# Optimization experiments

Measured on AMD Instinct MI355X. Metric: run time of the kernel, lower is better.

Reference implementation:

```python
import jax, jax.numpy as jnp
import numpy as np

D_MODEL = 1024
N_HEADS = 16
HEAD_DIM = D_MODEL // N_HEADS
SEQ_LEN = 2048
D_FF = 4 * D_MODEL
LCC_SCALE = 0.1
LN_EPS = 1e-5
NORM_EPS = 1e-12  # F.normalize eps


def _layer_norm(x, g, b):
    mu = jnp.mean(x, axis=-1, keepdims=True)
    var = jnp.mean(jnp.square(x - mu), axis=-1, keepdims=True)
    return (x - mu) * jax.lax.rsqrt(var + LN_EPS) * g + b


def setup_inputs() -> dict:
    key = jax.random.key(0)
    ks = jax.random.split(key, 8)
    s = 0.02  # weight init scale
    return {
        "x": jax.random.normal(ks[0], (SEQ_LEN, D_MODEL), jnp.float32),
        "lcc_values": jax.random.uniform(ks[1], (SEQ_LEN,), jnp.float32),
        "w_qkv": jax.random.normal(ks[2], (D_MODEL, 3 * D_MODEL), jnp.float32) * s,
        "b_qkv": jnp.zeros((3 * D_MODEL,), jnp.float32),
        "w_out": jax.random.normal(ks[3], (D_MODEL, D_MODEL), jnp.float32) * s,
        "b_out": jnp.zeros((D_MODEL,), jnp.float32),
        "ln1_g": jnp.ones((D_MODEL,), jnp.float32),
        "ln1_b": jnp.zeros((D_MODEL,), jnp.float32),
        "ln2_g": jnp.ones((D_MODEL,), jnp.float32),
        "ln2_b": jnp.zeros((D_MODEL,), jnp.float32),
        "w_ff1": jax.random.normal(ks[4], (D_MODEL, D_FF), jnp.float32) * s,
        "b_ff1": jnp.zeros((D_FF,), jnp.float32),
        "w_ff2": jax.random.normal(ks[5], (D_FF, D_MODEL), jnp.float32) * s,
        "b_ff2": jnp.zeros((D_MODEL,), jnp.float32),
    }


def reference(x, lcc_values, w_qkv, b_qkv, w_out, b_out, ln1_g, ln1_b,
              ln2_g, ln2_b, w_ff1, b_ff1, w_ff2, b_ff2):
    L = x.shape[0]
    scaling = HEAD_DIM ** -0.5

    normed = _layer_norm(x, ln1_g, ln1_b)
    qkv = normed @ w_qkv + b_qkv                      # [L, 3D]
    qkv = qkv.reshape(L, 3, N_HEADS, HEAD_DIM)
    q = jnp.transpose(qkv[:, 0], (1, 0, 2))           # [H, L, d]
    k = jnp.transpose(qkv[:, 1], (1, 0, 2))
    v = jnp.transpose(qkv[:, 2], (1, 0, 2))

    # cosine attention: L2-normalize q, k
    q = q / jnp.maximum(jnp.linalg.norm(q, axis=-1, keepdims=True), NORM_EPS)
    k = k / jnp.maximum(jnp.linalg.norm(k, axis=-1, keepdims=True), NORM_EPS)
    q = q * scaling

    scores = jnp.einsum('hld,hmd->hlm', q, k)         # [H, L, L]
    bias = (lcc_values[:, None] + lcc_values[None, :]) * 0.5 * LCC_SCALE
    scores = jnp.clip(scores + bias[None], -10.0, 10.0)
    probs = jax.nn.softmax(scores, axis=-1)

    attn = jnp.einsum('hlm,hmd->hld', probs, v)       # [H, L, d]
    attn = jnp.transpose(attn, (1, 0, 2)).reshape(L, D_MODEL)
    x = x + (attn @ w_out + b_out)

    normed2 = _layer_norm(x, ln2_g, ln2_b)
    h = jax.nn.gelu(normed2 @ w_ff1 + b_ff1, approximate=False)
    x = x + (h @ w_ff2 + b_ff2)
    return x
```

## Files before the change

kernel.cpp:

```cpp
#include <hip/hip_runtime.h>
#include <hip/hip_bf16.h>

#define D_MODEL 1024
#define SEQ 2048
#define NH 16
#define HD 64
#define DFF 4096

typedef __attribute__((ext_vector_type(8))) __bf16 bf16x8;
typedef __attribute__((ext_vector_type(4))) float f32x4;

__device__ __forceinline__ unsigned short f2bf(float f) {
    union { float f; unsigned u; } v; v.f = f;
    unsigned r = v.u + 0x7fffu + ((v.u >> 16) & 1u);
    return (unsigned short)(r >> 16);
}
__device__ __forceinline__ unsigned pack2(float a, float b) {
    return (unsigned)f2bf(a) | ((unsigned)f2bf(b) << 16);
}
__device__ __forceinline__ float bf2f(unsigned short u) {
    union { unsigned u; float f; } v; v.u = ((unsigned)u) << 16;
    return v.f;
}
__device__ __forceinline__ bf16x8 ld_frag(const unsigned short* p) {
    union { uint4 u; bf16x8 b; } c;
    c.u = *(const uint4*)p;
    return c.b;
}
__device__ __forceinline__ void load16(const float* p, float* v) {
#pragma unroll
    for (int i = 0; i < 4; i++) {
        float4 f = ((const float4*)p)[i];
        v[4*i+0]=f.x; v[4*i+1]=f.y; v[4*i+2]=f.z; v[4*i+3]=f.w;
    }
}

typedef __attribute__((address_space(3))) unsigned lds_u32;
typedef const __attribute__((address_space(1))) unsigned glob_u32;
__device__ __forceinline__ void gl_lds16(const unsigned short* g, unsigned short* l) {
    __builtin_amdgcn_global_load_lds((glob_u32*)g, (lds_u32*)l, 16, 0, 0);
}

#define MFMA16(a,b,c) __builtin_amdgcn_mfma_f32_16x16x32_bf16(a,b,c,0,0,0)

__global__ __launch_bounds__(256) void wcast_t(const float* __restrict__ W,
                                               unsigned short* __restrict__ Wt,
                                               int K, int N) {
    __shared__ unsigned short lt[64][72];
    int t = threadIdx.x;
    int nb = blockIdx.x, kb = blockIdx.y;
    int r = t >> 2, c0 = (t & 3) << 4;
    const float* src = W + (size_t)(kb*64 + r) * N + nb*64 + c0;
    float4 f0 = ((const float4*)src)[0];
    float4 f1 = ((const float4*)src)[1];
    float4 f2 = ((const float4*)src)[2];
    float4 f3 = ((const float4*)src)[3];
    unsigned* dst = (unsigned*)&lt[r][c0];
    dst[0]=pack2(f0.x,f0.y); dst[1]=pack2(f0.z,f0.w);
    dst[2]=pack2(f1.x,f1.y); dst[3]=pack2(f1.z,f1.w);
    dst[4]=pack2(f2.x,f2.y); dst[5]=pack2(f2.z,f2.w);
    dst[6]=pack2(f3.x,f3.y); dst[7]=pack2(f3.z,f3.w);
    __syncthreads();
    int n_ = t >> 2, k0 = (t & 3) << 4;
    unsigned obuf[8];
#pragma unroll
    for (int i = 0; i < 8; i++)
        obuf[i] = (unsigned)lt[k0 + 2*i][n_] | ((unsigned)lt[k0 + 2*i + 1][n_] << 16);
    unsigned short* out = Wt + (size_t)(nb*64 + n_) * K + kb*64 + k0;
    ((uint4*)out)[0] = *(uint4*)&obuf[0];
    ((uint4*)out)[1] = *(uint4*)&obuf[4];
}

__global__ __launch_bounds__(256) void ln_kernel(const float* __restrict__ x,
                                                 const float* __restrict__ g,
                                                 const float* __restrict__ b,
                                                 unsigned short* __restrict__ out) {
    int row = blockIdx.x, t = threadIdx.x;
    float4 v = ((const float4*)(x + (size_t)row * D_MODEL))[t];
    float s  = v.x + v.y + v.z + v.w;
    float sq = v.x*v.x + v.y*v.y + v.z*v.z + v.w*v.w;
#pragma unroll
    for (int m = 1; m < 64; m <<= 1) { s += __shfl_xor(s, m, 64); sq += __shfl_xor(sq, m, 64); }
    __shared__ float ls[4], lq[4];
    int wave = t >> 6, lane = t & 63;
    if (lane == 0) { ls[wave] = s; lq[wave] = sq; }
    __syncthreads();
    s  = ls[0]+ls[1]+ls[2]+ls[3];
    sq = lq[0]+lq[1]+lq[2]+lq[3];
    float mu  = s * (1.0f / D_MODEL);
    float var = sq * (1.0f / D_MODEL) - mu * mu;
    float rs  = rsqrtf(var + 1e-5f);
    int c = t * 4;
    float y0 = (v.x - mu) * rs * g[c+0] + b[c+0];
    float y1 = (v.y - mu) * rs * g[c+1] + b[c+1];
    float y2 = (v.z - mu) * rs * g[c+2] + b[c+2];
    float y3 = (v.w - mu) * rs * g[c+3] + b[c+3];
    unsigned* o = (unsigned*)(out + (size_t)row * D_MODEL + c);
    o[0] = pack2(y0, y1); o[1] = pack2(y2, y3);
}

template<int NP>
__global__ __launch_bounds__(256) void reduce_k(const float* __restrict__ res,
                                                const float* __restrict__ bias,
                                                const unsigned short* __restrict__ parts,
                                                float* __restrict__ out,
                                                int MN, int Ndiv4) {
    int i = blockIdx.x * 256 + threadIdx.x;
    float4 r = ((const float4*)res)[i];
    float4 b = ((const float4*)bias)[i & (Ndiv4 - 1)];
    r.x += b.x; r.y += b.y; r.z += b.z; r.w += b.w;
#pragma unroll
    for (int p = 0; p < NP; p++) {
        ushort4 u = ((const ushort4*)(parts + (size_t)p * MN))[i];
        r.x += bf2f(u.x); r.y += bf2f(u.y); r.z += bf2f(u.z); r.w += bf2f(u.w);
    }
    ((float4*)out)[i] = r;
}

template<int TM, int TN, int SPLITK, int GELU, int RES, int OUTBF, int PART>
__global__ __launch_bounds__(256) void gemm_bt(const unsigned short* __restrict__ A,
                                               const unsigned short* __restrict__ Bt,
                                               const float* __restrict__ bias,
                                               const float* __restrict__ res,
                                               void* __restrict__ C,
                                               int M, int N, int K) {
    constexpr int AI = TM / 32;
    constexpr int BI = TN / 32;
    constexpr int MI = TM / 32;
    constexpr int NI = TN / 32;
    constexpr int HALF = (TM + TN) * 64;
    __shared__ unsigned short smem[2 * HALF];
    int t = threadIdx.x;
    int bn = blockIdx.x, bm = blockIdx.y;
    int kz = (SPLITK > 1) ? blockIdx.z : 0;
    int KS = K / SPLITK;
    int K0 = kz * KS;
    int wave = t >> 6, lane = t & 63;
    int quad = lane >> 4, lr = lane & 15;

    const unsigned short* pa[AI];
    int aoff[AI];
#pragma unroll
    for (int i = 0; i < AI; i++) {
        int rl = wave*(TM/4) + i*8 + (lane >> 3);
        int ss = (lane & 7) ^ (rl & 7);
        pa[i] = A + (size_t)(bm*TM + rl) * K + K0 + ss*8;
        aoff[i] = (wave*(TM/4) + i*8) * 64;
    }
    const unsigned short* pb[BI];
    int boff[BI];
#pragma unroll
    for (int i = 0; i < BI; i++) {
        int rl = wave*(TN/4) + i*8 + (lane >> 3);
        int ss = (lane & 7) ^ (rl & 7);
        pb[i] = Bt + (size_t)(bn*TN + rl) * K + K0 + ss*8;
        boff[i] = TM*64 + (wave*(TN/4) + i*8) * 64;
    }

    int wr = (wave >> 1) * (TM/2), wc = (wave & 1) * (TN/2);
    int foA[2][MI], foB[2][NI];
#pragma unroll
    for (int i = 0; i < MI; i++) {
        int row = wr + i*16 + lr;
        foA[0][i] = row*64 + ((quad     ^ (row & 7)))*8;
        foA[1][i] = row*64 + (((quad+4) ^ (row & 7)))*8;
    }
#pragma unroll
    for (int j = 0; j < NI; j++) {
        int row = wc + j*16 + lr;
        foB[0][j] = TM*64 + row*64 + ((quad     ^ (row & 7)))*8;
        foB[1][j] = TM*64 + row*64 + (((quad+4) ^ (row & 7)))*8;
    }

    f32x4 z = {0.f, 0.f, 0.f, 0.f};
    f32x4 acc[MI][NI];
#pragma unroll
    for (int i = 0; i < MI; i++)
#pragma unroll
        for (int j = 0; j < NI; j++) acc[i][j] = z;

#pragma unroll
    for (int i = 0; i < AI; i++) gl_lds16(pa[i], smem + aoff[i]);
#pragma unroll
    for (int i = 0; i < BI; i++) gl_lds16(pb[i], smem + boff[i]);

    int bo = 0;
    for (int kk = 0; kk < KS; kk += 64) {
        __syncthreads();
        if (kk + 64 < KS) {
            int nb = bo ^ HALF;
#pragma unroll
            for (int i = 0; i < AI; i++) gl_lds16(pa[i] + kk + 64, smem + nb + aoff[i]);
#pragma unroll
            for (int i = 0; i < BI; i++) gl_lds16(pb[i] + kk + 64, smem + nb + boff[i]);
        }
#pragma unroll
        for (int h = 0; h < 2; h++) {
            bf16x8 af[MI], bfr[NI];
#pragma unroll
            for (int i = 0; i < MI; i++) af[i]  = ld_frag(smem + bo + foA[h][i]);
#pragma unroll
            for (int j = 0; j < NI; j++) bfr[j] = ld_frag(smem + bo + foB[h][j]);
#pragma unroll
            for (int i = 0; i < MI; i++)
#pragma unroll
                for (int j = 0; j < NI; j++)
                    acc[i][j] = MFMA16(af[i], bfr[j], acc[i][j]);
        }
        bo ^= HALF;
    }

    if (PART) {
        unsigned short* P = (unsigned short*)C + (size_t)kz * M * N;
#pragma unroll
        for (int i = 0; i < MI; i++)
#pragma unroll
            for (int j = 0; j < NI; j++) {
                int row0 = bm*TM + wr + i*16 + quad*4;
                int col  = bn*TN + wc + j*16 + lr;
#pragma unroll
                for (int r = 0; r < 4; r++)
                    P[(size_t)(row0 + r) * N + col] = f2bf(acc[i][j][r]);
            }
    } else {
#pragma unroll
        for (int i = 0; i < MI; i++)
#pragma unroll
            for (int j = 0; j < NI; j++) {
                int row0 = bm*TM + wr + i*16 + quad*4;
                int col  = bn*TN + wc + j*16 + lr;
                float bv = bias[col];
#pragma unroll
                for (int r = 0; r < 4; r++) {
                    float v = acc[i][j][r] + bv;
                    if (RES)  v += res[(size_t)(row0 + r) * N + col];
                    if (GELU) v = 0.5f * v * (1.0f + erff(v * 0.70710678118654752f));
                    if (OUTBF) ((unsigned short*)C)[(size_t)(row0 + r) * N + col] = f2bf(v);
                    else       ((float*)C)[(size_t)(row0 + r) * N + col] = v;
                }
            }
    }
}

__global__ __launch_bounds__(256) void qkv_post(const float* __restrict__ qkv,
                                                unsigned short* __restrict__ qn,
                                                unsigned short* __restrict__ kn,
                                                unsigned short* __restrict__ vt) {
    __shared__ unsigned short lv[64][72];
    int h = blockIdx.x, lb = blockIdx.y;
    int t = threadIdx.x;
    int lloc = t >> 2, seg = (t & 3) << 4;
    int lg = lb*64 + lloc;
    const float* row = qkv + (size_t)lg * 3072;
    float vq[16], vk[16], vv[16];
    load16(row + h*64 + seg, vq);
    load16(row + 1024 + h*64 + seg, vk);
    load16(row + 2048 + h*64 + seg, vv);
    float sq = 0.f, sk = 0.f;
#pragma unroll
    for (int i = 0; i < 16; i++) { sq += vq[i]*vq[i]; sk += vk[i]*vk[i]; }
    sq += __shfl_xor(sq, 1, 64); sq += __shfl_xor(sq, 2, 64);
    sk += __shfl_xor(sk, 1, 64); sk += __shfl_xor(sk, 2, 64);
    float scq = 0.125f / fmaxf(sqrtf(sq), 1e-12f);
    float sck = 1.0f   / fmaxf(sqrtf(sk), 1e-12f);
    unsigned* oq = (unsigned*)(qn + ((size_t)h*SEQ + lg)*HD + seg);
    unsigned* ok = (unsigned*)(kn + ((size_t)h*SEQ + lg)*HD + seg);
#pragma unroll
    for (int i = 0; i < 8; i++) {
        oq[i] = pack2(vq[2*i]*scq, vq[2*i+1]*scq);
        ok[i] = pack2(vk[2*i]*sck, vk[2*i+1]*sck);
    }
    unsigned* lvp = (unsigned*)&lv[lloc][seg];
#pragma unroll
    for (int i = 0; i < 8; i++) lvp[i] = pack2(vv[2*i], vv[2*i+1]);
    __syncthreads();
    int dloc = t >> 2, l0 = (t & 3) << 4;
    unsigned obuf[8];
#pragma unroll
    for (int i = 0; i < 8; i++)
        obuf[i] = (unsigned)lv[l0 + 2*i][dloc] | ((unsigned)lv[l0 + 2*i + 1][dloc] << 16);
    unsigned short* ov = vt + ((size_t)h*HD + dloc)*SEQ + lb*64 + l0;
    ((uint4*)ov)[0] = *(uint4*)&obuf[0];
    ((uint4*)ov)[1] = *(uint4*)&obuf[4];
}

__global__ __launch_bounds__(256) void attn_kernel(const unsigned short* __restrict__ qn,
                                                   const unsigned short* __restrict__ kn,
                                                   const unsigned short* __restrict__ vt,
                                                   const float* __restrict__ lcc,
                                                   unsigned short* __restrict__ attn) {
    __shared__ unsigned short lQ[64][72];
    __shared__ unsigned short lK[64][72];
    __shared__ unsigned short lV[64][72];
    __shared__ unsigned short lP[64][72];
    __shared__ float lL[SEQ];
    int h = blockIdx.x, qb = blockIdx.y;
    int t = threadIdx.x;
    int rl = t >> 2, c0 = (t & 3) << 4;
    const unsigned short* pq = qn + ((size_t)h*SEQ + qb*64 + rl)*HD + c0;
    *(uint4*)&lQ[rl][c0]     = ((const uint4*)pq)[0];
    *(uint4*)&lQ[rl][c0 + 8] = ((const uint4*)pq)[1];
    for (int i = t; i < SEQ; i += 256) lL[i] = 0.05f * lcc[i];
    __syncthreads();
    int wave = t >> 6, lane = t & 63, quad = lane >> 4, lr = lane & 15;
    float lqv[4];
#pragma unroll
    for (int r = 0; r < 4; r++) lqv[r] = lL[qb*64 + wave*16 + quad*4 + r];
    bf16x8 aq0 = ld_frag(&lQ[wave*16 + lr][quad*8]);
    bf16x8 aq1 = ld_frag(&lQ[wave*16 + lr][32 + quad*8]);
    f32x4 z = {0.f, 0.f, 0.f, 0.f};
    f32x4 oacc[4]; oacc[0]=z; oacc[1]=z; oacc[2]=z; oacc[3]=z;
    float den[4] = {0.f, 0.f, 0.f, 0.f};

    for (int kb = 0; kb < SEQ/64; kb++) {
        __syncthreads();
        const unsigned short* pk = kn + ((size_t)h*SEQ + kb*64 + rl)*HD + c0;
        uint4 k0v = ((const uint4*)pk)[0], k1v = ((const uint4*)pk)[1];
        const unsigned short* pv = vt + ((size_t)h*HD + rl)*SEQ + kb*64 + c0;
        uint4 v0v = ((const uint4*)pv)[0], v1v = ((const uint4*)pv)[1];
        *(uint4*)&lK[rl][c0]     = k0v; *(uint4*)&lK[rl][c0 + 8] = k1v;
        *(uint4*)&lV[rl][c0]     = v0v; *(uint4*)&lV[rl][c0 + 8] = v1v;
        __syncthreads();
#pragma unroll
        for (int j = 0; j < 4; j++) {
            bf16x8 b0 = ld_frag(&lK[j*16 + lr][quad*8]);
            bf16x8 b1 = ld_frag(&lK[j*16 + lr][32 + quad*8]);
            f32x4 s = z;
            s = MFMA16(aq0, b0, s);
            s = MFMA16(aq1, b1, s);
            float lm = lL[kb*64 + j*16 + lr];
#pragma unroll
            for (int r = 0; r < 4; r++) {
                float sv = s[r] + lqv[r] + lm;
                sv = fminf(fmaxf(sv, -10.f), 10.f);
                float p = __expf(sv);
                den[r] += p;
                lP[wave*16 + quad*4 + r][j*16 + lr] = f2bf(p);
            }
        }
        bf16x8 ap0 = ld_frag(&lP[wave*16 + lr][quad*8]);
        bf16x8 ap1 = ld_frag(&lP[wave*16 + lr][32 + quad*8]);
#pragma unroll
        for (int j2 = 0; j2 < 4; j2++) {
            bf16x8 b0 = ld_frag(&lV[j2*16 + lr][quad*8]);
            bf16x8 b1 = ld_frag(&lV[j2*16 + lr][32 + quad*8]);
            oacc[j2] = MFMA16(ap0, b0, oacc[j2]);
            oacc[j2] = MFMA16(ap1, b1, oacc[j2]);
        }
    }
#pragma unroll
    for (int r = 0; r < 4; r++)
#pragma unroll
        for (int m = 1; m < 16; m <<= 1) den[r] += __shfl_xor(den[r], m, 64);
#pragma unroll
    for (int j2 = 0; j2 < 4; j2++)
#pragma unroll
        for (int r = 0; r < 4; r++) {
            float ov = oacc[j2][r] / den[r];
            int rowg = qb*64 + wave*16 + quad*4 + r;
            int colg = h*64 + j2*16 + lr;
            attn[(size_t)rowg * D_MODEL + colg] = f2bf(ov);
        }
}

extern "C" void kernel_launch(void* const* d_in, const int* in_sizes, int n_in,
                              void* d_out, int out_size, void* d_ws, size_t ws_size,
                              hipStream_t stream) {
    const float* x      = (const float*)d_in[0];
    const float* lcc    = (const float*)d_in[1];
    const float* w_qkv  = (const float*)d_in[2];
    const float* b_qkv  = (const float*)d_in[3];
    const float* w_out  = (const float*)d_in[4];
    const float* b_out  = (const float*)d_in[5];
    const float* ln1_g  = (const float*)d_in[6];
    const float* ln1_b  = (const float*)d_in[7];
    const float* ln2_g  = (const float*)d_in[8];
    const float* ln2_b  = (const float*)d_in[9];
    const float* w_ff1  = (const float*)d_in[10];
    const float* b_ff1  = (const float*)d_in[11];
    const float* w_ff2  = (const float*)d_in[12];
    const float* b_ff2  = (const float*)d_in[13];

    char* ws = (char*)d_ws;
    unsigned short* wtq  = (unsigned short*)(ws);
    unsigned short* wto  = (unsigned short*)(ws + 6291456);
    unsigned short* wtf1 = (unsigned short*)(ws + 8388608);
    unsigned short* wtf2 = (unsigned short*)(ws + 16777216);
    unsigned short* xn   = (unsigned short*)(ws + 25165824);
    float*          qkvb = (float*)(ws + 29360128);
    float*          x1   = (float*)(ws + 29360128);
    unsigned short* hbuf = (unsigned short*)(ws + 37748736);
    unsigned short* pOP  = (unsigned short*)(ws + 37748736);
    unsigned short* qnb  = (unsigned short*)(ws + 54525952);
    unsigned short* knb  = (unsigned short*)(ws + 58720256);
    unsigned short* vtb  = (unsigned short*)(ws + 62914560);
    unsigned short* pFF2 = (unsigned short*)(ws);
    unsigned short* attnb = xn;
    unsigned short* x2n  = qnb;
    float* outp = (float*)d_out;

    wcast_t<<<dim3(48, 16), 256, 0, stream>>>(w_qkv, wtq, 1024, 3072);
    wcast_t<<<dim3(16, 16), 256, 0, stream>>>(w_out, wto, 1024, 1024);
    wcast_t<<<dim3(64, 16), 256, 0, stream>>>(w_ff1, wtf1, 1024, 4096);
    wcast_t<<<dim3(16, 64), 256, 0, stream>>>(w_ff2, wtf2, 4096, 1024);
    ln_kernel<<<SEQ, 256, 0, stream>>>(x, ln1_g, ln1_b, xn);
    gemm_bt<128,64,1,0,0,0,0><<<dim3(48, 16), 256, 0, stream>>>(xn, wtq, b_qkv, nullptr, qkvb, SEQ, 3072, 1024);
    qkv_post<<<dim3(16, 32), 256, 0, stream>>>(qkvb, qnb, knb, vtb);
    attn_kernel<<<dim3(16, 32), 256, 0, stream>>>(qnb, knb, vtb, lcc, attnb);
    gemm_bt<128,64,2,0,0,0,1><<<dim3(16, 16, 2), 256, 0, stream>>>(attnb, wto, nullptr, nullptr, pOP, SEQ, 1024, 1024);
    reduce_k<2><<<SEQ*D_MODEL/1024, 256, 0, stream>>>(x, b_out, pOP, x1, SEQ*D_MODEL, D_MODEL/4);
    ln_kernel<<<SEQ, 256, 0, stream>>>(x1, ln2_g, ln2_b, x2n);
    gemm_bt<128,64,1,1,0,1,0><<<dim3(64, 16), 256, 0, stream>>>(x2n, wtf1, b_ff1, nullptr, hbuf, SEQ, 4096, 1024);
    gemm_bt<128,64,4,0,0,0,1><<<dim3(16, 16, 4), 256, 0, stream>>>(hbuf, wtf2, nullptr, nullptr, pFF2, SEQ, 1024, 4096);
    reduce_k<4><<<SEQ*D_MODEL/1024, 256, 0, stream>>>(x1, b_ff2, pFF2, outp, SEQ*D_MODEL, D_MODEL/4);
}
```

Baseline: 294.5 us.

## Split attention over key dimension and add combine kernel

Attention now splits the key sequence into two halves across a third grid dimension. Each block writes unnormalized fp32 numerators and row denominators to workspace, and a new combine kernel sums the halves, normalizes and writes bf16 output. This doubles the number of attention blocks to improve GPU occupancy, at the cost of extra workspace traffic and one more launch. GEMM and reduce templates are wrapped in named non-template kernels, with no intended speed effect.

```diff
diff --git a/kernel.cpp b/kernel.cpp
--- a/kernel.cpp
+++ b/kernel.cpp
@@ -100,11 +100,11 @@
 }
 
 template<int NP>
-__global__ __launch_bounds__(256) void reduce_k(const float* __restrict__ res,
-                                                const float* __restrict__ bias,
-                                                const unsigned short* __restrict__ parts,
-                                                float* __restrict__ out,
-                                                int MN, int Ndiv4) {
+__device__ __forceinline__ void reduce_body(const float* __restrict__ res,
+                                            const float* __restrict__ bias,
+                                            const unsigned short* __restrict__ parts,
+                                            float* __restrict__ out,
+                                            int MN, int Ndiv4) {
     int i = blockIdx.x * 256 + threadIdx.x;
     float4 r = ((const float4*)res)[i];
     float4 b = ((const float4*)bias)[i & (Ndiv4 - 1)];
@@ -116,14 +116,24 @@
     }
     ((float4*)out)[i] = r;
 }
+__global__ __launch_bounds__(256) void reduce_op(const float* res, const float* bias,
+                                                 const unsigned short* parts, float* out,
+                                                 int MN, int Ndiv4) {
+    reduce_body<2>(res, bias, parts, out, MN, Ndiv4);
+}
+__global__ __launch_bounds__(256) void reduce_ff2(const float* res, const float* bias,
+                                                  const unsigned short* parts, float* out,
+                                                  int MN, int Ndiv4) {
+    reduce_body<4>(res, bias, parts, out, MN, Ndiv4);
+}
 
 template<int TM, int TN, int SPLITK, int GELU, int RES, int OUTBF, int PART>
-__global__ __launch_bounds__(256) void gemm_bt(const unsigned short* __restrict__ A,
-                                               const unsigned short* __restrict__ Bt,
-                                               const float* __restrict__ bias,
-                                               const float* __restrict__ res,
-                                               void* __restrict__ C,
-                                               int M, int N, int K) {
+__device__ __forceinline__ void gemm_body(const unsigned short* __restrict__ A,
+                                          const unsigned short* __restrict__ Bt,
+                                          const float* __restrict__ bias,
+                                          const float* __restrict__ res,
+                                          void* __restrict__ C,
+                                          int M, int N, int K) {
     constexpr int AI = TM / 32;
     constexpr int BI = TN / 32;
     constexpr int MI = TM / 32;
@@ -240,6 +250,23 @@
                 }
             }
     }
+}
+
+__global__ __launch_bounds__(256) void k_gemm_qkv(const unsigned short* A, const unsigned short* Bt,
+                                                  const float* bias, float* C, int M, int N, int K) {
+    gemm_body<128,64,1,0,0,0,0>(A, Bt, bias, nullptr, C, M, N, K);
+}
+__global__ __launch_bounds__(256) void k_gemm_op(const unsigned short* A, const unsigned short* Bt,
+                                                 unsigned short* C, int M, int N, int K) {
+    gemm_body<128,64,2,0,0,0,1>(A, Bt, nullptr, nullptr, C, M, N, K);
+}
+__global__ __launch_bounds__(256) void k_gemm_ff1(const unsigned short* A, const unsigned short* Bt,
+                                                  const float* bias, unsigned short* C, int M, int N, int K) {
+    gemm_body<128,64,1,1,0,1,0>(A, Bt, bias, nullptr, C, M, N, K);
+}
+__global__ __launch_bounds__(256) void k_gemm_ff2(const unsigned short* A, const unsigned short* Bt,
+                                                  unsigned short* C, int M, int N, int K) {
+    gemm_body<128,64,4,0,0,0,1>(A, Bt, nullptr, nullptr, C, M, N, K);
 }
 
 __global__ __launch_bounds__(256) void qkv_post(const float* __restrict__ qkv,
@@ -284,39 +311,45 @@
     ((uint4*)ov)[1] = *(uint4*)&obuf[4];
 }
 
+#define KSPLIT 2
+#define KTILES (SEQ / 64 / KSPLIT)
 __global__ __launch_bounds__(256) void attn_kernel(const unsigned short* __restrict__ qn,
                                                    const unsigned short* __restrict__ kn,
                                                    const unsigned short* __restrict__ vt,
                                                    const float* __restrict__ lcc,
-                                                   unsigned short* __restrict__ attn) {
+                                                   float* __restrict__ num_ws,
+                                                   float* __restrict__ den_ws) {
     __shared__ unsigned short lQ[64][72];
     __shared__ unsigned short lK[64][72];
     __shared__ unsigned short lV[64][72];
     __shared__ unsigned short lP[64][72];
-    __shared__ float lL[SEQ];
-    int h = blockIdx.x, qb = blockIdx.y;
+    __shared__ float lL[SEQ / KSPLIT];
+    int h = blockIdx.x, qb = blockIdx.y, kz = blockIdx.z;
     int t = threadIdx.x;
     int rl = t >> 2, c0 = (t & 3) << 4;
     const unsigned short* pq = qn + ((size_t)h*SEQ + qb*64 + rl)*HD + c0;
     *(uint4*)&lQ[rl][c0]     = ((const uint4*)pq)[0];
     *(uint4*)&lQ[rl][c0 + 8] = ((const uint4*)pq)[1];
-    for (int i = t; i < SEQ; i += 256) lL[i] = 0.05f * lcc[i];
+    for (int i = t; i < SEQ/KSPLIT; i += 256) lL[i] = 0.05f * lcc[kz*(SEQ/KSPLIT) + i];
     __syncthreads();
     int wave = t >> 6, lane = t & 63, quad = lane >> 4, lr = lane & 15;
     float lqv[4];
 #pragma unroll
-    for (int r = 0; r < 4; r++) lqv[r] = lL[qb*64 + wave*16 + quad*4 + r];
+    for (int r = 0; r < 4; r++) lqv[r] = 0.05f * lcc[qb*64 + wave*16 + quad*4 + r];
     bf16x8 aq0 = ld_frag(&lQ[wave*16 + lr][quad*8]);
     bf16x8 aq1 = ld_frag(&lQ[wave*16 + lr][32 + quad*8]);
     f32x4 z = {0.f, 0.f, 0.f, 0.f};
     f32x4 oacc[4]; oacc[0]=z; oacc[1]=z; oacc[2]=z; oacc[3]=z;
     float den[4] = {0.f, 0.f, 0.f, 0.f};
 
-    for (int kb = 0; kb < SEQ/64; kb++) {
+    const unsigned short* kn0 = kn + (size_t)h*SEQ*HD + (size_t)kz*(SEQ/KSPLIT)*HD;
+    const unsigned short* vt0 = vt + (size_t)h*HD*SEQ + kz*(SEQ/KSPLIT);
+
+    for (int kb = 0; kb < KTILES; kb++) {
         __syncthreads();
-        const unsigned short* pk = kn + ((size_t)h*SEQ + kb*64 + rl)*HD + c0;
+        const unsigned short* pk = kn0 + (size_t)(kb*64 + rl)*HD + c0;
         uint4 k0v = ((const uint4*)pk)[0], k1v = ((const uint4*)pk)[1];
-        const unsigned short* pv = vt + ((size_t)h*HD + rl)*SEQ + kb*64 + c0;
+        const unsigned short* pv = vt0 + (size_t)rl*SEQ + kb*64 + c0;
         uint4 v0v = ((const uint4*)pv)[0], v1v = ((const uint4*)pv)[1];
         *(uint4*)&lK[rl][c0]     = k0v; *(uint4*)&lK[rl][c0 + 8] = k1v;
         *(uint4*)&lV[rl][c0]     = v0v; *(uint4*)&lV[rl][c0 + 8] = v1v;
@@ -352,15 +385,42 @@
     for (int r = 0; r < 4; r++)
 #pragma unroll
         for (int m = 1; m < 16; m <<= 1) den[r] += __shfl_xor(den[r], m, 64);
+
+    float* nump = num_ws + (((size_t)(h*32 + qb)) * KSPLIT + kz) * 4096;
 #pragma unroll
     for (int j2 = 0; j2 < 4; j2++)
 #pragma unroll
-        for (int r = 0; r < 4; r++) {
-            float ov = oacc[j2][r] / den[r];
-            int rowg = qb*64 + wave*16 + quad*4 + r;
-            int colg = h*64 + j2*16 + lr;
-            attn[(size_t)rowg * D_MODEL + colg] = f2bf(ov);
-        }
+        for (int r = 0; r < 4; r++)
+            nump[(wave*16 + quad*4 + r) * 64 + j2*16 + lr] = oacc[j2][r];
+    if (lr == 0) {
+        float* denp = den_ws + (((size_t)(h*32 + qb)) * KSPLIT + kz) * 64;
+#pragma unroll
+        for (int r = 0; r < 4; r++) denp[wave*16 + quad*4 + r] = den[r];
+    }
+}
+
+__global__ __launch_bounds__(256) void attn_comb(const float* __restrict__ num_ws,
+                                                 const float* __restrict__ den_ws,
+                                                 unsigned short* __restrict__ attn) {
+    int hq = blockIdx.x;
+    int h = hq >> 5, qb = hq & 31;
+    int t = threadIdx.x;
+    int row = t >> 2, col0 = (t & 3) << 4;
+    const float* n0 = num_ws + ((size_t)hq * KSPLIT) * 4096 + row*64 + col0;
+    const float* n1 = n0 + 4096;
+    float d = den_ws[(size_t)hq * KSPLIT * 64 + row] + den_ws[((size_t)hq * KSPLIT + 1) * 64 + row];
+    float inv = 1.0f / d;
+    unsigned ob[8];
+#pragma unroll
+    for (int i = 0; i < 4; i++) {
+        float4 a = ((const float4*)n0)[i];
+        float4 b = ((const float4*)n1)[i];
+        ob[2*i]   = pack2((a.x + b.x) * inv, (a.y + b.y) * inv);
+        ob[2*i+1] = pack2((a.z + b.z) * inv, (a.w + b.w) * inv);
+    }
+    unsigned short* op = attn + (size_t)(qb*64 + row) * D_MODEL + h*64 + col0;
+    ((uint4*)op)[0] = *(uint4*)&ob[0];
+    ((uint4*)op)[1] = *(uint4*)&ob[4];
 }
 
 extern "C" void kernel_launch(void* const* d_in, const int* in_sizes, int n_in,
@@ -389,6 +449,8 @@
     unsigned short* xn   = (unsigned short*)(ws + 25165824);
     float*          qkvb = (float*)(ws + 29360128);
     float*          x1   = (float*)(ws + 29360128);
+    float*          numw = (float*)(ws + 29360128);
+    float*          denw = (float*)(ws + 46137344);
     unsigned short* hbuf = (unsigned short*)(ws + 37748736);
     unsigned short* pOP  = (unsigned short*)(ws + 37748736);
     unsigned short* qnb  = (unsigned short*)(ws + 54525952);
@@ -399,18 +461,20 @@
     unsigned short* x2n  = qnb;
     float* outp = (float*)d_out;
 
+
     wcast_t<<<dim3(48, 16), 256, 0, stream>>>(w_qkv, wtq, 1024, 3072);
     wcast_t<<<dim3(16, 16), 256, 0, stream>>>(w_out, wto, 1024, 1024);
     wcast_t<<<dim3(64, 16), 256, 0, stream>>>(w_ff1, wtf1, 1024, 4096);
     wcast_t<<<dim3(16, 64), 256, 0, stream>>>(w_ff2, wtf2, 4096, 1024);
     ln_kernel<<<SEQ, 256, 0, stream>>>(x, ln1_g, ln1_b, xn);
-    gemm_bt<128,64,1,0,0,0,0><<<dim3(48, 16), 256, 0, stream>>>(xn, wtq, b_qkv, nullptr, qkvb, SEQ, 3072, 1024);
+    k_gemm_qkv<<<dim3(48, 16), 256, 0, stream>>>(xn, wtq, b_qkv, qkvb, SEQ, 3072, 1024);
     qkv_post<<<dim3(16, 32), 256, 0, stream>>>(qkvb, qnb, knb, vtb);
-    attn_kernel<<<dim3(16, 32), 256, 0, stream>>>(qnb, knb, vtb, lcc, attnb);
-    gemm_bt<128,64,2,0,0,0,1><<<dim3(16, 16, 2), 256, 0, stream>>>(attnb, wto, nullptr, nullptr, pOP, SEQ, 1024, 1024);
-    reduce_k<2><<<SEQ*D_MODEL/1024, 256, 0, stream>>>(x, b_out, pOP, x1, SEQ*D_MODEL, D_MODEL/4);
+    attn_kernel<<<dim3(16, 32, KSPLIT), 256, 0, stream>>>(qnb, knb, vtb, lcc, numw, denw);
+    attn_comb<<<512, 256, 0, stream>>>(numw, denw, attnb);
+    k_gemm_op<<<dim3(16, 16, 2), 256, 0, stream>>>(attnb, wto, pOP, SEQ, 1024, 1024);
+    reduce_op<<<SEQ*D_MODEL/1024, 256, 0, stream>>>(x, b_out, pOP, x1, SEQ*D_MODEL, D_MODEL/4);
     ln_kernel<<<SEQ, 256, 0, stream>>>(x1, ln2_g, ln2_b, x2n);
-    gemm_bt<128,64,1,1,0,1,0><<<dim3(64, 16), 256, 0, stream>>>(x2n, wtf1, b_ff1, nullptr, hbuf, SEQ, 4096, 1024);
-    gemm_bt<128,64,4,0,0,0,1><<<dim3(16, 16, 4), 256, 0, stream>>>(hbuf, wtf2, nullptr, nullptr, pFF2, SEQ, 1024, 4096);
-    reduce_k<4><<<SEQ*D_MODEL/1024, 256, 0, stream>>>(x1, b_ff2, pFF2, outp, SEQ*D_MODEL, D_MODEL/4);
-}
+    k_gemm_ff1<<<dim3(64, 16), 256, 0, stream>>>(x2n, wtf1, b_ff1, hbuf, SEQ, 4096, 1024);
+    k_gemm_ff2<<<dim3(16, 16, 4), 256, 0, stream>>>(hbuf, wtf2, pFF2, SEQ, 1024, 4096);
+    reduce_ff2<<<SEQ*D_MODEL/1024, 256, 0, stream>>>(x1, b_ff2, pFF2, outp, SEQ*D_MODEL, D_MODEL/4);
+}
```

After: 283.1 us. 1.04x faster.
